# Kernel optimization log

Measured on AMD Instinct MI355X. Metric: run time of the kernel, lower is better.

## Reference

```python
import jax, jax.numpy as jnp
import numpy as np
from jax import lax

K1, K2 = 0.01, 0.03
VALUE_RANGE = 1.0
DN = ('NCHW', 'OIHW', 'NCHW')


def gaussian_kernel(size, sigma):
    t = jnp.arange(size, dtype=jnp.float32) - (size - 1) / 2.0
    k = jnp.exp(-(t ** 2) / (2.0 * sigma ** 2))
    return k / k.sum()  # (K,)


def sep_conv(x, kernel):
    # x: (N,C,H,W); kernel: (C,1,K) depthwise separable gaussian, VALID padding
    C = kernel.shape[0]
    kh = kernel[:, :, :, None]  # (C,1,K,1) -> conv along H
    kw = kernel[:, :, None, :]  # (C,1,1,K) -> conv along W
    x = lax.conv_general_dilated(x, kh, (1, 1), 'VALID', dimension_numbers=DN,
                                 feature_group_count=C)
    x = lax.conv_general_dilated(x, kw, (1, 1), 'VALID', dimension_numbers=DN,
                                 feature_group_count=C)
    return x


def ssim_cs(x, y, kernel):
    # returns per-(N,C) SSIM and CS, spatial mean
    c1 = (K1 * VALUE_RANGE) ** 2
    c2 = (K2 * VALUE_RANGE) ** 2
    mu_x = sep_conv(x, kernel)
    mu_y = sep_conv(y, kernel)
    mu_xx = mu_x ** 2
    mu_yy = mu_y ** 2
    mu_xy = mu_x * mu_y
    sigma_xx = sep_conv(x * x, kernel) - mu_xx
    sigma_yy = sep_conv(y * y, kernel) - mu_yy
    sigma_xy = sep_conv(x * y, kernel) - mu_xy
    cs = (2 * sigma_xy + c2) / (sigma_xx + sigma_yy + c2)
    ss = (2 * mu_xy + c1) / (mu_xx + mu_yy + c1) * cs
    return ss.mean(axis=(2, 3)), cs.mean(axis=(2, 3))  # (N,C) each


def avg_pool2(x):
    # stride-2 2x2 average pool; H,W chosen even at every scale so ceil_mode moot
    N, C, H, W = x.shape
    return x.reshape(N, C, H // 2, 2, W // 2, 2).mean(axis=(3, 5))


def setup_inputs() -> dict:
    key = jax.random.key(0)
    kx, ky = jax.random.split(key)
    x = jax.random.uniform(kx, (8, 3, 512, 512), dtype=jnp.float32)
    y = jax.random.uniform(ky, (8, 3, 512, 512), dtype=jnp.float32)
    kernel = jnp.tile(gaussian_kernel(11, 1.5)[None, None, :], (3, 1, 1))  # (C,1,K)
    weights = jnp.array([0.0448, 0.2856, 0.3001, 0.2363, 0.1333], dtype=jnp.float32)
    return {"x": x, "y": y, "kernel": kernel, "weights": weights}


def reference(x, y, kernel, weights):
    m = weights.shape[0]
    css = []
    for i in range(m):
        if i > 0:
            x = avg_pool2(x)
            y = avg_pool2(y)
        ss, cs = ssim_cs(x, y, kernel)
        css.append(jnp.maximum(ss if i + 1 == m else cs, 0.0))
    msss = jnp.stack(css, axis=-1) ** weights  # (N,C,M)
    msss = msss.prod(axis=-1).mean(axis=-1)    # (N,)
    return msss.mean()  # reduction='mean'
```

## Files before the change

kernel.cpp:

```cpp
#include <hip/hip_runtime.h>
#include <hip/hip_fp16.h>

#define NCH 24
#define KS 11
#define TH 32
#define TW 64
#define IWC 76

typedef float f32x2 __attribute__((ext_vector_type(2)));
typedef __half2 hbuf_t[TH][IWC];

template<bool GUARD>
__device__ __forceinline__ void v_pass_pk(
    const float* __restrict__ Xp, const float* __restrict__ Yp,
    const float* __restrict__ k, int H, int W, int gx0, int gy0, int tid,
    __half2 (*vb01)[IWC], __half2 (*vb23)[IWC])
{
    if (tid < 3 * IWC) {
        const int c  = tid % IWC;
        const int rg = tid / IWC;
        const int r0 = rg * 11;
        const int gc = gx0 + c;
        const bool cok = (!GUARD) || (gc < W);

        f32x2 a01[11], a23[11];
#pragma unroll
        for (int i = 0; i < 11; ++i) {
            a01[i] = (f32x2){0.f, 0.f};
            a23[i] = (f32x2){0.f, 0.f};
        }

        const float* xptr = Xp + (size_t)(gy0 + r0) * W + gc;
        const float* yptr = Yp + (size_t)(gy0 + r0) * W + gc;

        float xr[10], yr[10];
#pragma unroll
        for (int i = 0; i < 10; ++i) {
            if (GUARD) {
                const int gy = gy0 + r0 + i;
                xr[i] = 0.f; yr[i] = 0.f;
                if (cok && gy < H) { xr[i] = xptr[0]; yr[i] = yptr[0]; }
            } else {
                xr[i] = xptr[0]; yr[i] = yptr[0];
            }
            xptr += W; yptr += W;
        }

#pragma unroll
        for (int ri = 0; ri < 21; ++ri) {
            const int s = ri % 10;
            const float xv = xr[s], yv = yr[s];
            if (ri + 10 < 21) {
                if (GUARD) {
                    const int gy = gy0 + r0 + ri + 10;
                    xr[s] = 0.f; yr[s] = 0.f;
                    if (cok && gy < H) { xr[s] = xptr[0]; yr[s] = yptr[0]; }
                } else {
                    xr[s] = xptr[0]; yr[s] = yptr[0];
                }
                xptr += W; yptr += W;
            }

            f32x2 vxy, vsx;
            vxy.x = xv; vxy.y = yv;
            vsx.x = fmaf(yv, yv, xv * xv);
            vsx.y = xv * yv;
#pragma unroll
            for (int rv = 0; rv < 11; ++rv) {
                if (rv < (ri > 10 ? ri - 10 : 0)) continue;
                if (rv > (ri < 10 ? ri : 10)) continue;
                const float kt = k[ri - rv];
                f32x2 kv; kv.x = kt; kv.y = kt;
                a01[rv] += kv * vxy;
                a23[rv] += kv * vsx;
            }
        }
#pragma unroll
        for (int rv = 0; rv < 11; ++rv) {
            const int r = r0 + rv;
            if (r < TH) {
                vb01[r][c] = __floats2half2_rn(a01[rv].x, a01[rv].y);
                vb23[r][c] = __floats2half2_rn(a23[rv].x, a23[rv].y);
            }
        }
    }
}

template<bool GUARD>
__device__ __forceinline__ void h_pass_pk(
    const float* __restrict__ k, int H, int W, int gx0, int gy0, int tid,
    const __half2 (*vb01)[IWC], const __half2 (*vb23)[IWC],
    float& ss_acc, float& cs_acc)
{
    const float c1 = 1e-4f, c2 = 9e-4f;
    const int row = tid >> 3;
    const int cg  = tid & 7;
    const int c0  = cg * 8;
    const bool rowok = (!GUARD) || ((gy0 + row) <= (H - KS));

    f32x2 h01[8], h23[8];
#pragma unroll
    for (int j = 0; j < 8; ++j) {
        h01[j] = (f32x2){0.f, 0.f};
        h23[j] = (f32x2){0.f, 0.f};
    }

#pragma unroll
    for (int fp = 0; fp < 2; ++fp) {
        const uint4* p = reinterpret_cast<const uint4*>(
            fp == 0 ? &vb01[row][c0] : &vb23[row][c0]);
        f32x2* h2 = (fp == 0) ? h01 : h23;
#pragma unroll
        for (int b = 0; b < 5; ++b) {
            uint4 q = p[b];
            unsigned qs[4] = {q.x, q.y, q.z, q.w};
#pragma unroll
            for (int u = 0; u < 4; ++u) {
                const int i = 4 * b + u;
                if (i > 18) continue;
                __half2 hv = *reinterpret_cast<const __half2*>(&qs[u]);
                float2 f = __half22float2(hv);
                f32x2 w; w.x = f.x; w.y = f.y;
#pragma unroll
                for (int j = 0; j < 8; ++j) {
                    const int t = i - j;
                    if (t >= 0 && t < KS) {
                        f32x2 kv; kv.x = k[t]; kv.y = k[t];
                        h2[j] += kv * w;
                    }
                }
            }
        }
    }

#pragma unroll
    for (int j = 0; j < 8; ++j) {
        bool ok = rowok && ((!GUARD) || ((gx0 + c0 + j) <= (W - KS)));
        if (ok) {
            float mx = h01[j].x, my = h01[j].y;
            float S = h23[j].x, vxy = h23[j].y;
            float mxx = mx * mx, myy = my * my, mxy = mx * my;
            float msum = mxx + myy;
            float sxy = vxy - mxy, ssum = S - msum;
            float cs = (2.f * sxy + c2) * __builtin_amdgcn_rcpf(ssum + c2);
            float ssv = (2.f * mxy + c1) * __builtin_amdgcn_rcpf(msum + c1) * cs;
            ss_acc += ssv; cs_acc += cs;
        }
    }
}

__device__ __forceinline__ void block_reduce_store(
    float ss_acc, float cs_acc, int tid, float* red, float* slot)
{
    for (int off = 32; off > 0; off >>= 1) {
        ss_acc += __shfl_down(ss_acc, off);
        cs_acc += __shfl_down(cs_acc, off);
    }
    const int wave = tid >> 6;
    if ((tid & 63) == 0) { red[wave * 2] = ss_acc; red[wave * 2 + 1] = cs_acc; }
    __syncthreads();
    if (tid == 0) {
        slot[0] = red[0] + red[2] + red[4] + red[6];
        slot[1] = red[1] + red[3] + red[5] + red[7];
    }
}

__global__ __launch_bounds__(256, 6) void ssim_scale0_kernel(
    const float* __restrict__ X, const float* __restrict__ Y,
    const float* __restrict__ kern, float* __restrict__ part,
    float* __restrict__ X1, float* __restrict__ Y1,
    float* __restrict__ X2, float* __restrict__ Y2,
    float* __restrict__ X3, float* __restrict__ Y3,
    float* __restrict__ X4, float* __restrict__ Y4)
{
    const int H = 512, W = 512;
    const int nc  = blockIdx.z;
    const int ch  = nc % 3;
    const int gx0 = blockIdx.x * TW;
    const int gy0 = blockIdx.y * TH;
    const int tid = threadIdx.x;

    __shared__ __align__(16) __half2 vb01[TH][IWC];
    __shared__ __align__(16) __half2 vb23[TH][IWC];
    __shared__ float red[8];

    float k[KS];
#pragma unroll
    for (int t = 0; t < KS; ++t) k[t] = kern[ch * KS + t];

    const float* Xp = X + (size_t)nc * H * W;
    const float* Yp = Y + (size_t)nc * H * W;

    const bool guard = (gx0 + IWC > W) || (gy0 + TH + 11 > H);
    if (guard) v_pass_pk<true >(Xp, Yp, k, H, W, gx0, gy0, tid, vb01, vb23);
    else       v_pass_pk<false>(Xp, Yp, k, H, W, gx0, gy0, tid, vb01, vb23);

    float plx[2], ply[2];
    {
        const int W2 = W >> 1;
#pragma unroll
        for (int i = 0; i < 2; ++i) {
            int p = tid + i * 256;
            int pr = p >> 5, pc = p & 31;
            int sr = gy0 + 2 * pr, sc = gx0 + 2 * pc;
            const float* xb = Xp + (size_t)sr * W + sc;
            const float* yb = Yp + (size_t)sr * W + sc;
            float2 xa = *reinterpret_cast<const float2*>(xb);
            float2 xc = *reinterpret_cast<const float2*>(xb + W);
            float2 ya = *reinterpret_cast<const float2*>(yb);
            float2 yc = *reinterpret_cast<const float2*>(yb + W);
            plx[i] = 0.25f * (xa.x + xa.y + xc.x + xc.y);
            ply[i] = 0.25f * (ya.x + ya.y + yc.x + yc.y);
            size_t di = (size_t)nc * W2 * W2 + (size_t)((gy0 >> 1) + pr) * W2 + ((gx0 >> 1) + pc);
            X1[di] = plx[i];
            Y1[di] = ply[i];
        }
    }
    __syncthreads();

    float ss_acc = 0.f, cs_acc = 0.f;
    if (guard) h_pass_pk<true >(k, H, W, gx0, gy0, tid, vb01, vb23, ss_acc, cs_acc);
    else       h_pass_pk<false>(k, H, W, gx0, gy0, tid, vb01, vb23, ss_acc, cs_acc);
    __syncthreads();

    float* pb = (float*)vb01;
    pb[tid]        = plx[0];
    pb[tid + 256]  = plx[1];
    pb[512 + tid]  = ply[0];
    pb[768 + tid]  = ply[1];
    __syncthreads();
    {
        const int W4 = W >> 2;
        int a = tid >> 7, p = tid & 127;
        int pr = p >> 4, pc = p & 15;
        const float* src = pb + a * 512;
        float v = 0.25f * (src[(2*pr)*32 + 2*pc] + src[(2*pr)*32 + 2*pc + 1] +
                           src[(2*pr+1)*32 + 2*pc] + src[(2*pr+1)*32 + 2*pc + 1]);
        pb[1024 + a * 128 + p] = v;
        size_t di = (size_t)nc * W4 * W4 + (size_t)((gy0 >> 2) + pr) * W4 + ((gx0 >> 2) + pc);
        (a ? Y2 : X2)[di] = v;
    }
    __syncthreads();
    if (tid < 64) {
        const int W8 = W >> 3;
        int a = tid >> 5, p = tid & 31;
        int pr = p >> 3, pc = p & 7;
        const float* src = pb + 1024 + a * 128;
        float v = 0.25f * (src[(2*pr)*16 + 2*pc] + src[(2*pr)*16 + 2*pc + 1] +
                           src[(2*pr+1)*16 + 2*pc] + src[(2*pr+1)*16 + 2*pc + 1]);
        pb[1280 + a * 32 + p] = v;
        size_t di = (size_t)nc * W8 * W8 + (size_t)((gy0 >> 3) + pr) * W8 + ((gx0 >> 3) + pc);
        (a ? Y3 : X3)[di] = v;
    }
    __syncthreads();
    if (tid < 16) {
        const int W16 = W >> 4;
        int a = tid >> 3, p = tid & 7;
        int pr = p >> 2, pc = p & 3;
        const float* src = pb + 1280 + a * 32;
        float v = 0.25f * (src[(2*pr)*8 + 2*pc] + src[(2*pr)*8 + 2*pc + 1] +
                           src[(2*pr+1)*8 + 2*pc] + src[(2*pr+1)*8 + 2*pc + 1]);
        size_t di = (size_t)nc * W16 * W16 + (size_t)((gy0 >> 4) + pr) * W16 + ((gx0 >> 4) + pc);
        (a ? Y4 : X4)[di] = v;
    }

    int t = blockIdx.y * gridDim.x + blockIdx.x;
    block_reduce_store(ss_acc, cs_acc, tid, red,
                       part + ((size_t)nc * (gridDim.x * gridDim.y) + t) * 2);
}

__global__ __launch_bounds__(256, 6) void ssim_rest_kernel(
    const float* __restrict__ x1, const float* __restrict__ y1,
    const float* __restrict__ x2, const float* __restrict__ y2,
    const float* __restrict__ x3, const float* __restrict__ y3,
    const float* __restrict__ x4, const float* __restrict__ y4,
    const float* __restrict__ kern, float* __restrict__ part)
{
    const int z = blockIdx.z;
    const int tid = threadIdx.x;

    int img, bx, by, H, poff, nt, gw;
    const float *Xs, *Ys;
    if (z < 768)       { int r = z;        img = r >> 5; int t = r & 31; bx = t & 3; by = t >> 2; H = 256; Xs = x1; Ys = y1; poff = 6144; nt = 32; gw = 4; }
    else if (z < 960)  { int r = z - 768;  img = r >> 3; int t = r & 7;  bx = t & 1; by = t >> 1; H = 128; Xs = x2; Ys = y2; poff = 7680; nt = 8;  gw = 2; }
    else if (z < 1008) { int r = z - 960;  img = r >> 1; bx = 0; by = r & 1;         H = 64;  Xs = x3; Ys = y3; poff = 8064; nt = 2;  gw = 1; }
    else               { img = z - 1008;   bx = 0; by = 0;                           H = 32;  Xs = x4; Ys = y4; poff = 8160; nt = 1;  gw = 1; }
    const int W = H;
    const int gx0 = bx * TW, gy0 = by * TH;
    const int ch = img % 3;

    __shared__ __align__(16) __half2 vb01[TH][IWC];
    __shared__ __align__(16) __half2 vb23[TH][IWC];
    __shared__ float red[8];

    float k[KS];
#pragma unroll
    for (int t = 0; t < KS; ++t) k[t] = kern[ch * KS + t];

    const float* Xp = Xs + (size_t)img * H * W;
    const float* Yp = Ys + (size_t)img * H * W;

    const bool guard = (gx0 + IWC > W) || (gy0 + TH + 11 > H);
    if (guard) v_pass_pk<true >(Xp, Yp, k, H, W, gx0, gy0, tid, vb01, vb23);
    else       v_pass_pk<false>(Xp, Yp, k, H, W, gx0, gy0, tid, vb01, vb23);
    __syncthreads();

    float ss_acc = 0.f, cs_acc = 0.f;
    if (guard) h_pass_pk<true >(k, H, W, gx0, gy0, tid, vb01, vb23, ss_acc, cs_acc);
    else       h_pass_pk<false>(k, H, W, gx0, gy0, tid, vb01, vb23, ss_acc, cs_acc);

    int tl = by * gw + bx;
    block_reduce_store(ss_acc, cs_acc, tid, red,
                       part + poff + ((size_t)img * nt + tl) * 2);
}

__global__ __launch_bounds__(256) void finalize_kernel(
    const float* __restrict__ part, const float* __restrict__ wts,
    float* __restrict__ out)
{
    __shared__ float smean[NCH][5];
    __shared__ float prods[NCH];
    const int ntiles[5] = {128, 32, 8, 2, 1};
    const int bases[5]  = {0, 6144, 7680, 8064, 8160};
    const float counts[5] = {252004.f, 60516.f, 13924.f, 2916.f, 484.f};
    int tid = threadIdx.x;

    for (int p = tid; p < NCH * 5; p += blockDim.x) {
        int s = p % 5, nc = p / 5;
        int nt = ntiles[s];
        const float* base = part + bases[s] + (size_t)nc * nt * 2;
        int sel = (s == 4) ? 0 : 1;
        float acc = 0.f;
        for (int t = 0; t < nt; ++t) acc += base[t * 2 + sel];
        smean[nc][s] = acc / counts[s];
    }
    __syncthreads();
    if (tid < NCH) {
        float pr = 1.f;
#pragma unroll
        for (int s = 0; s < 5; ++s) {
            float v = fmaxf(smean[tid][s], 0.f);
            pr *= powf(v, wts[s]);
        }
        prods[tid] = pr;
    }
    __syncthreads();
    if (tid == 0) {
        float m = 0.f;
        for (int i = 0; i < NCH; ++i) m += prods[i];
        out[0] = m / (float)NCH;
    }
}

extern "C" void kernel_launch(void* const* d_in, const int* in_sizes, int n_in,
                              void* d_out, int out_size, void* d_ws, size_t ws_size,
                              hipStream_t stream)
{
    const float* x    = (const float*)d_in[0];
    const float* y    = (const float*)d_in[1];
    const float* kern = (const float*)d_in[2];
    const float* wts  = (const float*)d_in[3];
    float* out = (float*)d_out;
    float* ws  = (float*)d_ws;

    size_t o = 0;
    float* x1 = ws + o; o += (size_t)NCH * 256 * 256;
    float* y1 = ws + o; o += (size_t)NCH * 256 * 256;
    float* x2 = ws + o; o += (size_t)NCH * 128 * 128;
    float* y2 = ws + o; o += (size_t)NCH * 128 * 128;
    float* x3 = ws + o; o += (size_t)NCH * 64 * 64;
    float* y3 = ws + o; o += (size_t)NCH * 64 * 64;
    float* x4 = ws + o; o += (size_t)NCH * 32 * 32;
    float* y4 = ws + o; o += (size_t)NCH * 32 * 32;
    float* part = ws + o;

    ssim_scale0_kernel<<<dim3(8, 16, NCH), 256, 0, stream>>>(
        x, y, kern, part, x1, y1, x2, y2, x3, y3, x4, y4);

    ssim_rest_kernel<<<dim3(1, 1, 1032), 256, 0, stream>>>(
        x1, y1, x2, y2, x3, y3, x4, y4, kern, part);

    finalize_kernel<<<1, 256, 0, stream>>>(part, wts, out);
}
```

Measured before the change: 57.81 us.

## Store pooled pyramid as interleaved half2 and restructure pooling in shared memory

Pooled downsampled images for scales 1-4 are now stored as interleaved x/y half2 pairs instead of separate fp32 planes. This halves the intermediate write and read traffic and lets the later-scale vertical pass issue one load per pixel instead of two. The scale-0 pooling chain now keeps float2 pairs in dedicated shared buffers, which drops a barrier and the reuse of the conv buffer. In exchange the coarser scales lose precision from fp16 inputs, and the h-pass tap bound was changed from 18 to 17, which touches correctness if that last tap was needed.

```diff
diff --git a/kernel.cpp b/kernel.cpp
--- a/kernel.cpp
+++ b/kernel.cpp
@@ -8,10 +8,41 @@
 #define IWC 76
 
 typedef float f32x2 __attribute__((ext_vector_type(2)));
-typedef __half2 hbuf_t[TH][IWC];
+
+__device__ __forceinline__ void conv_acc(
+    f32x2* a01, f32x2* a23, const float* k, int ri, float xv, float yv)
+{
+    f32x2 vxy, vsx;
+    vxy.x = xv; vxy.y = yv;
+    vsx.x = fmaf(yv, yv, xv * xv);
+    vsx.y = xv * yv;
+#pragma unroll
+    for (int rv = 0; rv < 11; ++rv) {
+        if (rv < (ri > 10 ? ri - 10 : 0)) continue;
+        if (rv > (ri < 10 ? ri : 10)) continue;
+        const float kt = k[ri - rv];
+        f32x2 kv; kv.x = kt; kv.y = kt;
+        a01[rv] += kv * vxy;
+        a23[rv] += kv * vsx;
+    }
+}
+
+__device__ __forceinline__ void v_store(
+    __half2 (*vb01)[IWC], __half2 (*vb23)[IWC], int r0, int c,
+    const f32x2* a01, const f32x2* a23)
+{
+#pragma unroll
+    for (int rv = 0; rv < 11; ++rv) {
+        const int r = r0 + rv;
+        if (r < TH) {
+            vb01[r][c] = __floats2half2_rn(a01[rv].x, a01[rv].y);
+            vb23[r][c] = __floats2half2_rn(a23[rv].x, a23[rv].y);
+        }
+    }
+}
 
 template<bool GUARD>
-__device__ __forceinline__ void v_pass_pk(
+__device__ __forceinline__ void v_pass_f32(
     const float* __restrict__ Xp, const float* __restrict__ Yp,
     const float* __restrict__ k, int H, int W, int gx0, int gy0, int tid,
     __half2 (*vb01)[IWC], __half2 (*vb23)[IWC])
@@ -25,10 +56,7 @@
 
         f32x2 a01[11], a23[11];
 #pragma unroll
-        for (int i = 0; i < 11; ++i) {
-            a01[i] = (f32x2){0.f, 0.f};
-            a23[i] = (f32x2){0.f, 0.f};
-        }
+        for (int i = 0; i < 11; ++i) { a01[i] = (f32x2){0.f,0.f}; a23[i] = (f32x2){0.f,0.f}; }
 
         const float* xptr = Xp + (size_t)(gy0 + r0) * W + gc;
         const float* yptr = Yp + (size_t)(gy0 + r0) * W + gc;
@@ -60,29 +88,61 @@
                 }
                 xptr += W; yptr += W;
             }
-
-            f32x2 vxy, vsx;
-            vxy.x = xv; vxy.y = yv;
-            vsx.x = fmaf(yv, yv, xv * xv);
-            vsx.y = xv * yv;
-#pragma unroll
-            for (int rv = 0; rv < 11; ++rv) {
-                if (rv < (ri > 10 ? ri - 10 : 0)) continue;
-                if (rv > (ri < 10 ? ri : 10)) continue;
-                const float kt = k[ri - rv];
-                f32x2 kv; kv.x = kt; kv.y = kt;
-                a01[rv] += kv * vxy;
-                a23[rv] += kv * vsx;
+            conv_acc(a01, a23, k, ri, xv, yv);
+        }
+        v_store(vb01, vb23, r0, c, a01, a23);
+    }
+}
+
+template<bool GUARD>
+__device__ __forceinline__ void v_pass_h2(
+    const __half2* __restrict__ XYp,
+    const float* __restrict__ k, int H, int W, int gx0, int gy0, int tid,
+    __half2 (*vb01)[IWC], __half2 (*vb23)[IWC])
+{
+    if (tid < 3 * IWC) {
+        const int c  = tid % IWC;
+        const int rg = tid / IWC;
+        const int r0 = rg * 11;
+        const int gc = gx0 + c;
+        const bool cok = (!GUARD) || (gc < W);
+
+        f32x2 a01[11], a23[11];
+#pragma unroll
+        for (int i = 0; i < 11; ++i) { a01[i] = (f32x2){0.f,0.f}; a23[i] = (f32x2){0.f,0.f}; }
+
+        const __half2* p = XYp + (size_t)(gy0 + r0) * W + gc;
+
+        __half2 hr[10];
+#pragma unroll
+        for (int i = 0; i < 10; ++i) {
+            if (GUARD) {
+                const int gy = gy0 + r0 + i;
+                hr[i] = __floats2half2_rn(0.f, 0.f);
+                if (cok && gy < H) hr[i] = p[0];
+            } else {
+                hr[i] = p[0];
             }
-        }
-#pragma unroll
-        for (int rv = 0; rv < 11; ++rv) {
-            const int r = r0 + rv;
-            if (r < TH) {
-                vb01[r][c] = __floats2half2_rn(a01[rv].x, a01[rv].y);
-                vb23[r][c] = __floats2half2_rn(a23[rv].x, a23[rv].y);
+            p += W;
+        }
+
+#pragma unroll
+        for (int ri = 0; ri < 21; ++ri) {
+            const int s = ri % 10;
+            float2 f = __half22float2(hr[s]);
+            if (ri + 10 < 21) {
+                if (GUARD) {
+                    const int gy = gy0 + r0 + ri + 10;
+                    hr[s] = __floats2half2_rn(0.f, 0.f);
+                    if (cok && gy < H) hr[s] = p[0];
+                } else {
+                    hr[s] = p[0];
+                }
+                p += W;
             }
-        }
+            conv_acc(a01, a23, k, ri, f.x, f.y);
+        }
+        v_store(vb01, vb23, r0, c, a01, a23);
     }
 }
 
@@ -100,10 +160,7 @@
 
     f32x2 h01[8], h23[8];
 #pragma unroll
-    for (int j = 0; j < 8; ++j) {
-        h01[j] = (f32x2){0.f, 0.f};
-        h23[j] = (f32x2){0.f, 0.f};
-    }
+    for (int j = 0; j < 8; ++j) { h01[j] = (f32x2){0.f,0.f}; h23[j] = (f32x2){0.f,0.f}; }
 
 #pragma unroll
     for (int fp = 0; fp < 2; ++fp) {
@@ -117,7 +174,7 @@
 #pragma unroll
             for (int u = 0; u < 4; ++u) {
                 const int i = 4 * b + u;
-                if (i > 18) continue;
+                if (i > 17) continue;
                 __half2 hv = *reinterpret_cast<const __half2*>(&qs[u]);
                 float2 f = __half22float2(hv);
                 f32x2 w; w.x = f.x; w.y = f.y;
@@ -168,10 +225,8 @@
 __global__ __launch_bounds__(256, 6) void ssim_scale0_kernel(
     const float* __restrict__ X, const float* __restrict__ Y,
     const float* __restrict__ kern, float* __restrict__ part,
-    float* __restrict__ X1, float* __restrict__ Y1,
-    float* __restrict__ X2, float* __restrict__ Y2,
-    float* __restrict__ X3, float* __restrict__ Y3,
-    float* __restrict__ X4, float* __restrict__ Y4)
+    __half2* __restrict__ XY1, __half2* __restrict__ XY2,
+    __half2* __restrict__ XY3, __half2* __restrict__ XY4)
 {
     const int H = 512, W = 512;
     const int nc  = blockIdx.z;
@@ -182,6 +237,9 @@
 
     __shared__ __align__(16) __half2 vb01[TH][IWC];
     __shared__ __align__(16) __half2 vb23[TH][IWC];
+    __shared__ float2 pl1[512];
+    __shared__ float2 pl2[128];
+    __shared__ float2 pl3[32];
     __shared__ float red[8];
 
     float k[KS];
@@ -192,10 +250,9 @@
     const float* Yp = Y + (size_t)nc * H * W;
 
     const bool guard = (gx0 + IWC > W) || (gy0 + TH + 11 > H);
-    if (guard) v_pass_pk<true >(Xp, Yp, k, H, W, gx0, gy0, tid, vb01, vb23);
-    else       v_pass_pk<false>(Xp, Yp, k, H, W, gx0, gy0, tid, vb01, vb23);
-
-    float plx[2], ply[2];
+    if (guard) v_pass_f32<true >(Xp, Yp, k, H, W, gx0, gy0, tid, vb01, vb23);
+    else       v_pass_f32<false>(Xp, Yp, k, H, W, gx0, gy0, tid, vb01, vb23);
+
     {
         const int W2 = W >> 1;
 #pragma unroll
@@ -209,11 +266,11 @@
             float2 xc = *reinterpret_cast<const float2*>(xb + W);
             float2 ya = *reinterpret_cast<const float2*>(yb);
             float2 yc = *reinterpret_cast<const float2*>(yb + W);
-            plx[i] = 0.25f * (xa.x + xa.y + xc.x + xc.y);
-            ply[i] = 0.25f * (ya.x + ya.y + yc.x + yc.y);
+            float px = 0.25f * (xa.x + xa.y + xc.x + xc.y);
+            float py = 0.25f * (ya.x + ya.y + yc.x + yc.y);
+            pl1[p] = make_float2(px, py);
             size_t di = (size_t)nc * W2 * W2 + (size_t)((gy0 >> 1) + pr) * W2 + ((gx0 >> 1) + pc);
-            X1[di] = plx[i];
-            Y1[di] = ply[i];
+            XY1[di] = __floats2half2_rn(px, py);
         }
     }
     __syncthreads();
@@ -221,47 +278,40 @@
     float ss_acc = 0.f, cs_acc = 0.f;
     if (guard) h_pass_pk<true >(k, H, W, gx0, gy0, tid, vb01, vb23, ss_acc, cs_acc);
     else       h_pass_pk<false>(k, H, W, gx0, gy0, tid, vb01, vb23, ss_acc, cs_acc);
-    __syncthreads();
-
-    float* pb = (float*)vb01;
-    pb[tid]        = plx[0];
-    pb[tid + 256]  = plx[1];
-    pb[512 + tid]  = ply[0];
-    pb[768 + tid]  = ply[1];
-    __syncthreads();
-    {
+
+    if (tid < 128) {
         const int W4 = W >> 2;
-        int a = tid >> 7, p = tid & 127;
-        int pr = p >> 4, pc = p & 15;
-        const float* src = pb + a * 512;
-        float v = 0.25f * (src[(2*pr)*32 + 2*pc] + src[(2*pr)*32 + 2*pc + 1] +
-                           src[(2*pr+1)*32 + 2*pc] + src[(2*pr+1)*32 + 2*pc + 1]);
-        pb[1024 + a * 128 + p] = v;
+        int pr = tid >> 4, pc = tid & 15;
+        float2 a = pl1[(2*pr)*32 + 2*pc],     b = pl1[(2*pr)*32 + 2*pc + 1];
+        float2 cfl = pl1[(2*pr+1)*32 + 2*pc], d = pl1[(2*pr+1)*32 + 2*pc + 1];
+        float vx = 0.25f * (a.x + b.x + cfl.x + d.x);
+        float vy = 0.25f * (a.y + b.y + cfl.y + d.y);
+        pl2[tid] = make_float2(vx, vy);
         size_t di = (size_t)nc * W4 * W4 + (size_t)((gy0 >> 2) + pr) * W4 + ((gx0 >> 2) + pc);
-        (a ? Y2 : X2)[di] = v;
-    }
-    __syncthreads();
-    if (tid < 64) {
+        XY2[di] = __floats2half2_rn(vx, vy);
+    }
+    __syncthreads();
+    if (tid < 32) {
         const int W8 = W >> 3;
-        int a = tid >> 5, p = tid & 31;
-        int pr = p >> 3, pc = p & 7;
-        const float* src = pb + 1024 + a * 128;
-        float v = 0.25f * (src[(2*pr)*16 + 2*pc] + src[(2*pr)*16 + 2*pc + 1] +
-                           src[(2*pr+1)*16 + 2*pc] + src[(2*pr+1)*16 + 2*pc + 1]);
-        pb[1280 + a * 32 + p] = v;
+        int pr = tid >> 3, pc = tid & 7;
+        float2 a = pl2[(2*pr)*16 + 2*pc],     b = pl2[(2*pr)*16 + 2*pc + 1];
+        float2 cfl = pl2[(2*pr+1)*16 + 2*pc], d = pl2[(2*pr+1)*16 + 2*pc + 1];
+        float vx = 0.25f * (a.x + b.x + cfl.x + d.x);
+        float vy = 0.25f * (a.y + b.y + cfl.y + d.y);
+        pl3[tid] = make_float2(vx, vy);
         size_t di = (size_t)nc * W8 * W8 + (size_t)((gy0 >> 3) + pr) * W8 + ((gx0 >> 3) + pc);
-        (a ? Y3 : X3)[di] = v;
-    }
-    __syncthreads();
-    if (tid < 16) {
+        XY3[di] = __floats2half2_rn(vx, vy);
+    }
+    __syncthreads();
+    if (tid < 8) {
         const int W16 = W >> 4;
-        int a = tid >> 3, p = tid & 7;
-        int pr = p >> 2, pc = p & 3;
-        const float* src = pb + 1280 + a * 32;
-        float v = 0.25f * (src[(2*pr)*8 + 2*pc] + src[(2*pr)*8 + 2*pc + 1] +
-                           src[(2*pr+1)*8 + 2*pc] + src[(2*pr+1)*8 + 2*pc + 1]);
+        int pr = tid >> 2, pc = tid & 3;
+        float2 a = pl3[(2*pr)*8 + 2*pc],     b = pl3[(2*pr)*8 + 2*pc + 1];
+        float2 cfl = pl3[(2*pr+1)*8 + 2*pc], d = pl3[(2*pr+1)*8 + 2*pc + 1];
+        float vx = 0.25f * (a.x + b.x + cfl.x + d.x);
+        float vy = 0.25f * (a.y + b.y + cfl.y + d.y);
         size_t di = (size_t)nc * W16 * W16 + (size_t)((gy0 >> 4) + pr) * W16 + ((gx0 >> 4) + pc);
-        (a ? Y4 : X4)[di] = v;
+        XY4[di] = __floats2half2_rn(vx, vy);
     }
 
     int t = blockIdx.y * gridDim.x + blockIdx.x;
@@ -270,21 +320,19 @@
 }
 
 __global__ __launch_bounds__(256, 6) void ssim_rest_kernel(
-    const float* __restrict__ x1, const float* __restrict__ y1,
-    const float* __restrict__ x2, const float* __restrict__ y2,
-    const float* __restrict__ x3, const float* __restrict__ y3,
-    const float* __restrict__ x4, const float* __restrict__ y4,
+    const __half2* __restrict__ xy1, const __half2* __restrict__ xy2,
+    const __half2* __restrict__ xy3, const __half2* __restrict__ xy4,
     const float* __restrict__ kern, float* __restrict__ part)
 {
     const int z = blockIdx.z;
     const int tid = threadIdx.x;
 
     int img, bx, by, H, poff, nt, gw;
-    const float *Xs, *Ys;
-    if (z < 768)       { int r = z;        img = r >> 5; int t = r & 31; bx = t & 3; by = t >> 2; H = 256; Xs = x1; Ys = y1; poff = 6144; nt = 32; gw = 4; }
-    else if (z < 960)  { int r = z - 768;  img = r >> 3; int t = r & 7;  bx = t & 1; by = t >> 1; H = 128; Xs = x2; Ys = y2; poff = 7680; nt = 8;  gw = 2; }
-    else if (z < 1008) { int r = z - 960;  img = r >> 1; bx = 0; by = r & 1;         H = 64;  Xs = x3; Ys = y3; poff = 8064; nt = 2;  gw = 1; }
-    else               { img = z - 1008;   bx = 0; by = 0;                           H = 32;  Xs = x4; Ys = y4; poff = 8160; nt = 1;  gw = 1; }
+    const __half2* XYs;
+    if (z < 768)       { int r = z;        img = r >> 5; int t = r & 31; bx = t & 3; by = t >> 2; H = 256; XYs = xy1; poff = 6144; nt = 32; gw = 4; }
+    else if (z < 960)  { int r = z - 768;  img = r >> 3; int t = r & 7;  bx = t & 1; by = t >> 1; H = 128; XYs = xy2; poff = 7680; nt = 8;  gw = 2; }
+    else if (z < 1008) { int r = z - 960;  img = r >> 1; bx = 0; by = r & 1;         H = 64;  XYs = xy3; poff = 8064; nt = 2;  gw = 1; }
+    else               { img = z - 1008;   bx = 0; by = 0;                           H = 32;  XYs = xy4; poff = 8160; nt = 1;  gw = 1; }
     const int W = H;
     const int gx0 = bx * TW, gy0 = by * TH;
     const int ch = img % 3;
@@ -297,12 +345,11 @@
 #pragma unroll
     for (int t = 0; t < KS; ++t) k[t] = kern[ch * KS + t];
 
-    const float* Xp = Xs + (size_t)img * H * W;
-    const float* Yp = Ys + (size_t)img * H * W;
+    const __half2* XYp = XYs + (size_t)img * H * W;
 
     const bool guard = (gx0 + IWC > W) || (gy0 + TH + 11 > H);
-    if (guard) v_pass_pk<true >(Xp, Yp, k, H, W, gx0, gy0, tid, vb01, vb23);
-    else       v_pass_pk<false>(Xp, Yp, k, H, W, gx0, gy0, tid, vb01, vb23);
+    if (guard) v_pass_h2<true >(XYp, k, H, W, gx0, gy0, tid, vb01, vb23);
+    else       v_pass_h2<false>(XYp, k, H, W, gx0, gy0, tid, vb01, vb23);
     __syncthreads();
 
     float ss_acc = 0.f, cs_acc = 0.f;
@@ -364,21 +411,17 @@
     float* ws  = (float*)d_ws;
 
     size_t o = 0;
-    float* x1 = ws + o; o += (size_t)NCH * 256 * 256;
-    float* y1 = ws + o; o += (size_t)NCH * 256 * 256;
-    float* x2 = ws + o; o += (size_t)NCH * 128 * 128;
-    float* y2 = ws + o; o += (size_t)NCH * 128 * 128;
-    float* x3 = ws + o; o += (size_t)NCH * 64 * 64;
-    float* y3 = ws + o; o += (size_t)NCH * 64 * 64;
-    float* x4 = ws + o; o += (size_t)NCH * 32 * 32;
-    float* y4 = ws + o; o += (size_t)NCH * 32 * 32;
+    __half2* xy1 = (__half2*)(ws + o); o += (size_t)NCH * 256 * 256;
+    __half2* xy2 = (__half2*)(ws + o); o += (size_t)NCH * 128 * 128;
+    __half2* xy3 = (__half2*)(ws + o); o += (size_t)NCH * 64 * 64;
+    __half2* xy4 = (__half2*)(ws + o); o += (size_t)NCH * 32 * 32;
     float* part = ws + o;
 
     ssim_scale0_kernel<<<dim3(8, 16, NCH), 256, 0, stream>>>(
-        x, y, kern, part, x1, y1, x2, y2, x3, y3, x4, y4);
+        x, y, kern, part, xy1, xy2, xy3, xy4);
 
     ssim_rest_kernel<<<dim3(1, 1, 1032), 256, 0, stream>>>(
-        x1, y1, x2, y2, x3, y3, x4, y4, kern, part);
+        xy1, xy2, xy3, xy4, kern, part);
 
     finalize_kernel<<<1, 256, 0, stream>>>(part, wts, out);
 }
```

Measured after the change: 56.62 us, median of 2. 1.02x faster.
